# Optimization experiments

Measured on AMD Instinct MI355X. Metric: run time of the kernel, lower is better.

Reference implementation:

```python
import jax, jax.numpy as jnp
import numpy as np


def setup_inputs() -> dict:
    key = jax.random.key(0)
    k_adj, k_ann, k_b = jax.random.split(key, 3)
    B, N, F = 8, 4096, 64
    # Adjacency: sparse-ish nonnegative matrix (TF version stores it as tf.sparse;
    raw = jax.random.uniform(k_adj, (B, N, N), dtype=jnp.float32)
    adjacent = jnp.where(raw > 0.95, raw, 0.0)
    annotations = jax.random.normal(k_ann, (B, N, F), dtype=jnp.float32)
    bias = jax.random.normal(k_b, (1, 1, F), dtype=jnp.float32)
    return {"adjacent": adjacent, "annotations": annotations, "bias": bias}


def reference(adjacent, annotations, bias):
    # Per-batch sparse @ dense matmul in TF == batched matmul here.
    # adjacent: [B,N,N], annotations: [B,N,F] -> [B,N,F]
    out = jnp.einsum('bnm,bmf->bnf', adjacent, annotations)
    return out + bias
```

## Files before the change

kernel.cpp:

```cpp
#include <hip/hip_runtime.h>
#include <stdint.h>

typedef __bf16 bf16x8 __attribute__((ext_vector_type(8)));
typedef float f32x16 __attribute__((ext_vector_type(16)));

#define NN 4096
#define FF 64
#define BM 32
#define BK 128
#define NSTEP (NN / BK)
#define NKB (NN / 16)

__device__ __forceinline__ unsigned short f2bf(float x) {
    unsigned int u = __builtin_bit_cast(unsigned int, x);
    unsigned int r = u + 0x7fffu + ((u >> 16) & 1u);
    return (unsigned short)(r >> 16);
}

__device__ __forceinline__ void gload16(const void* g, void* l) {
    __builtin_amdgcn_global_load_lds((const __attribute__((address_space(1))) void*)g,
                                     (__attribute__((address_space(3))) void*)l, 16, 0, 0);
}

__global__ __launch_bounds__(256) void annP_kernel(const float* __restrict__ ann,
                                                   unsigned short* __restrict__ annP) {
    int blk = blockIdx.x;
    int b = blk >> 6;
    int kb = (blk & 63) * 4 + (threadIdx.x >> 6);
    int f = threadIdx.x & 63;
    const float* src = ann + (size_t)(b * NN + kb * 16) * FF + f;
    unsigned short v[16];
#pragma unroll
    for (int kh = 0; kh < 16; ++kh) v[kh] = f2bf(src[(size_t)kh * FF]);
    unsigned int p[8];
#pragma unroll
    for (int i = 0; i < 8; ++i) p[i] = (unsigned)v[2 * i] | ((unsigned)v[2 * i + 1] << 16);
    uint4* dst = (uint4*)(annP + ((size_t)(b * NKB + kb) * 64 + f) * 16);
    dst[0] = make_uint4(p[0], p[1], p[2], p[3]);
    dst[1] = make_uint4(p[4], p[5], p[6], p[7]);
}

__global__ __launch_bounds__(128) void gconv_kernel(const float* __restrict__ A,
                                                    const unsigned short* __restrict__ annP,
                                                    const float* __restrict__ bias,
                                                    float* __restrict__ out) {
    __shared__ alignas(16) char lds[2][16384];

    int bi = blockIdx.x;
    int b = bi & 7;
    int n0 = (bi >> 3) << 5;
    int t = threadIdx.x, lane = t & 63, wf = t >> 6;
    int r = lane & 31, h = lane >> 5;

    const float* Ab = A + (size_t)b * NN * NN + (size_t)n0 * NN;

    const float* asrc[8];
#pragma unroll
    for (int j = 0; j < 8; ++j) {
        unsigned s = (unsigned)(j * 2048 + t * 16);
        unsigned row = s >> 9;
        unsigned q = ((s & 511u) ^ ((row & 15u) << 4)) >> 4;
        asrc[j] = Ab + (size_t)row * NN + q * 4;
    }
    auto STAGE = [&](int buf, int k0) {
        char* base = lds[buf];
#pragma unroll
        for (int j = 0; j < 8; ++j) gload16(asrc[j] + k0, base + j * 2048 + wf * 1024);
    };

    const unsigned short* bfp =
        annP + (size_t)b * NKB * 1024 + (size_t)(wf * 32 + r) * 16 + h * 8;

    unsigned rbase = (unsigned)(r * 512);
    unsigned swz = (unsigned)((r & 15) << 4);

    f32x16 acc = {};
    uint4 bfrag[8];

    STAGE(0, 0);
#pragma unroll 1
    for (int s = 0; s < NSTEP; ++s) {
        int cur = s & 1;
        asm volatile("s_waitcnt vmcnt(0)" ::: "memory");
        __builtin_amdgcn_s_barrier();
        asm volatile("" ::: "memory");

        int kb0 = s * 8;
#pragma unroll
        for (int kc = 0; kc < 8; ++kc)
            bfrag[kc] = *(const uint4*)(bfp + (size_t)(kb0 + kc) * 1024);

        if (s + 1 < NSTEP) STAGE(cur ^ 1, (s + 1) * BK);

        const char* bufA = lds[cur];
#pragma unroll
        for (int kc = 0; kc < 8; ++kc) {
            unsigned ao = rbase + (unsigned)(kc * 64 + h * 32);
            float4 a0 = *(const float4*)(bufA + (ao ^ swz));
            float4 a1 = *(const float4*)(bufA + ((ao + 16) ^ swz));
            bf16x8 af = {(__bf16)a0.x, (__bf16)a0.y, (__bf16)a0.z, (__bf16)a0.w,
                         (__bf16)a1.x, (__bf16)a1.y, (__bf16)a1.z, (__bf16)a1.w};
            acc = __builtin_amdgcn_mfma_f32_32x32x16_bf16(
                af, __builtin_bit_cast(bf16x8, bfrag[kc]), acc, 0, 0, 0);
        }
    }

    float bv = bias[wf * 32 + r];
    float* ob = out + ((size_t)(b * NN + n0)) * FF + wf * 32 + r;
#pragma unroll
    for (int e = 0; e < 16; ++e) {
        int rowl = (e & 3) + 8 * (e >> 2) + h * 4;
        ob[(size_t)rowl * FF] = acc[e] + bv;
    }
}

extern "C" void kernel_launch(void* const* d_in, const int* in_sizes, int n_in,
                              void* d_out, int out_size, void* d_ws, size_t ws_size,
                              hipStream_t stream) {
    const float* adj = (const float*)d_in[0];
    const float* ann = (const float*)d_in[1];
    const float* bias = (const float*)d_in[2];
    float* out = (float*)d_out;
    unsigned short* annP = (unsigned short*)d_ws;

    annP_kernel<<<dim3(8 * 64), dim3(256), 0, stream>>>(ann, annP);
    gconv_kernel<<<dim3(8 * (NN / BM)), dim3(128), 0, stream>>>(adj, annP, bias, out);
}
```

Baseline: 680.4 us.

## Deepen A-tile pipeline to a 4-stage LDS ring with partial vmcnt waits

Halves the K tile to 64 and uses four LDS buffers with a prefetch distance of three stages, in place of a two-buffer ring. Each step now waits with a partial vmcnt(12) instead of fully draining vmcnt, so more global-to-LDS loads stay in flight. The B fragments are double-buffered in registers, one step ahead. The intent is to hide global memory latency on the fp32 adjacency stream. The cost is twice as many barriers per K. The partial-wait counting also leaves a possible ordering risk in the tail steps, where fewer loads are issued.

```diff
diff --git a/kernel.cpp b/kernel.cpp
--- a/kernel.cpp
+++ b/kernel.cpp
@@ -7,7 +7,7 @@
 #define NN 4096
 #define FF 64
 #define BM 32
-#define BK 128
+#define BK 64
 #define NSTEP (NN / BK)
 #define NKB (NN / 16)
 
@@ -44,7 +44,7 @@
                                                     const unsigned short* __restrict__ annP,
                                                     const float* __restrict__ bias,
                                                     float* __restrict__ out) {
-    __shared__ alignas(16) char lds[2][16384];
+    __shared__ alignas(16) char lds[4][8192];
 
     int bi = blockIdx.x;
     int b = bi & 7;
@@ -54,55 +54,70 @@
 
     const float* Ab = A + (size_t)b * NN * NN + (size_t)n0 * NN;
 
-    const float* asrc[8];
+    const float* asrc[4];
 #pragma unroll
-    for (int j = 0; j < 8; ++j) {
-        unsigned s = (unsigned)(j * 2048 + t * 16);
-        unsigned row = s >> 9;
-        unsigned q = ((s & 511u) ^ ((row & 15u) << 4)) >> 4;
+    for (int j = 0; j < 4; ++j) {
+        unsigned p = (unsigned)(j * 2048 + t * 16);
+        unsigned row = p >> 8;
+        unsigned q = ((p & 255u) ^ ((row & 15u) << 4)) >> 4;
         asrc[j] = Ab + (size_t)row * NN + q * 4;
     }
     auto STAGE = [&](int buf, int k0) {
         char* base = lds[buf];
 #pragma unroll
-        for (int j = 0; j < 8; ++j) gload16(asrc[j] + k0, base + j * 2048 + wf * 1024);
+        for (int j = 0; j < 4; ++j) gload16(asrc[j] + k0, base + j * 2048 + wf * 1024);
     };
 
     const unsigned short* bfp =
         annP + (size_t)b * NKB * 1024 + (size_t)(wf * 32 + r) * 16 + h * 8;
 
-    unsigned rbase = (unsigned)(r * 512);
+    unsigned rbase = (unsigned)(r * 256);
     unsigned swz = (unsigned)((r & 15) << 4);
 
     f32x16 acc = {};
-    uint4 bfrag[8];
+    uint4 bfA[4], bfB[4];
 
-    STAGE(0, 0);
-#pragma unroll 1
-    for (int s = 0; s < NSTEP; ++s) {
-        int cur = s & 1;
-        asm volatile("s_waitcnt vmcnt(0)" ::: "memory");
-        __builtin_amdgcn_s_barrier();
-        asm volatile("" ::: "memory");
-
-        int kb0 = s * 8;
+    auto loadB = [&](uint4 (&bf)[4], int s) {
+        int kb0 = s * 4;
 #pragma unroll
-        for (int kc = 0; kc < 8; ++kc)
-            bfrag[kc] = *(const uint4*)(bfp + (size_t)(kb0 + kc) * 1024);
-
-        if (s + 1 < NSTEP) STAGE(cur ^ 1, (s + 1) * BK);
-
-        const char* bufA = lds[cur];
+        for (int kc = 0; kc < 4; ++kc)
+            bf[kc] = *(const uint4*)(bfp + (size_t)(kb0 + kc) * 1024);
+    };
+    auto compute = [&](const uint4 (&bf)[4], int s) {
+        const char* bufA = lds[s & 3];
 #pragma unroll
-        for (int kc = 0; kc < 8; ++kc) {
+        for (int kc = 0; kc < 4; ++kc) {
             unsigned ao = rbase + (unsigned)(kc * 64 + h * 32);
             float4 a0 = *(const float4*)(bufA + (ao ^ swz));
             float4 a1 = *(const float4*)(bufA + ((ao + 16) ^ swz));
             bf16x8 af = {(__bf16)a0.x, (__bf16)a0.y, (__bf16)a0.z, (__bf16)a0.w,
                          (__bf16)a1.x, (__bf16)a1.y, (__bf16)a1.z, (__bf16)a1.w};
             acc = __builtin_amdgcn_mfma_f32_32x32x16_bf16(
-                af, __builtin_bit_cast(bf16x8, bfrag[kc]), acc, 0, 0, 0);
+                af, __builtin_bit_cast(bf16x8, bf[kc]), acc, 0, 0, 0);
         }
+    };
+
+    STAGE(0, 0);
+    STAGE(1, BK);
+    STAGE(2, 2 * BK);
+    loadB(bfA, 0);
+
+#pragma unroll 1
+    for (int i = 0; i < NSTEP / 2; ++i) {
+        int s0 = 2 * i;
+        asm volatile("s_waitcnt vmcnt(12)" ::: "memory");
+        __builtin_amdgcn_s_barrier();
+        asm volatile("" ::: "memory");
+        if (s0 + 1 < NSTEP) loadB(bfB, s0 + 1);
+        if (s0 + 3 < NSTEP) STAGE((s0 + 3) & 3, (s0 + 3) * BK);
+        compute(bfA, s0);
+        int s1 = s0 + 1;
+        asm volatile("s_waitcnt vmcnt(12)" ::: "memory");
+        __builtin_amdgcn_s_barrier();
+        asm volatile("" ::: "memory");
+        if (s1 + 1 < NSTEP) loadB(bfA, s1 + 1);
+        if (s1 + 3 < NSTEP) STAGE((s1 + 3) & 3, (s1 + 3) * BK);
+        compute(bfB, s1);
     }
 
     float bv = bias[wf * 32 + r];
```

After: 717.9 us. 5.5% more time.
